# Optimization experiments

Measured on AMD Instinct MI355X. Metric: run time of the kernel, lower is better.

## Reference

```python
import jax, jax.numpy as jnp
import numpy as np

S, N, K = 8, 2048, 64          # snapshots, atoms, max neighbors (sum of max_num_neighs)
L = 20.0                        # periodic box length
R_CS, R_C = 6.0, 12.0           # smooth cutoff radii
M2 = 16                         # dim_sub_net


def _mlp(x, params, resnet=False):
    # DenseChainNet: Linear -> relu per layer; resnet skip when dims match or double (DeepMD style)
    for W, b in params:
        y = jax.nn.relu(x @ W + b)
        if resnet and y.shape[-1] == x.shape[-1]:
            y = y + x
        elif resnet and y.shape[-1] == 2 * x.shape[-1]:
            y = y + jnp.concatenate([x, x], axis=-1)
        x = y
    return x


def setup_inputs() -> dict:
    ks = jax.random.split(jax.random.key(0), 14)
    inputs = jax.random.uniform(ks[0], (S, N, 3), jnp.float32) * L
    input_types = jax.random.randint(ks[1], (S, N), 0, 2)
    nl = jax.random.randint(ks[2], (S, N, K), 0, N)
    neigh_list = jnp.where(jax.random.uniform(ks[3], (S, N, K)) < 0.2, -1, nl)  # -1 = padded neighbor

    def w(k, i, o):
        return jax.random.normal(k, (i, o), jnp.float32) / np.float32(np.sqrt(i))

    return {
        'inputs': inputs,
        'input_types': input_types,
        'neigh_list': neigh_list,
        'length': jnp.array([L, L, L], jnp.float32),
        # embed_species (species_dim [2,16,32])
        'ew0': w(ks[4], 2, 16), 'eb0': jnp.zeros((16,), jnp.float32),
        'ew1': w(ks[5], 16, 32), 'eb1': jnp.zeros((32,), jnp.float32),
        # fit_species (species_fit [32,32,31])
        'fw0': w(ks[6], 32, 32), 'fb0': jnp.zeros((32,), jnp.float32),
        'fw1': w(ks[7], 32, 31), 'fb1': jnp.zeros((31,), jnp.float32),
        # embed_net (descript_dim [32,64,128], resnet=True)
        'gw0': w(ks[8], 32, 64), 'gb0': jnp.zeros((64,), jnp.float32),
        'gw1': w(ks[9], 64, 128), 'gb1': jnp.zeros((128,), jnp.float32),
    }


def reference(inputs, input_types, neigh_list, length,
              ew0, eb0, ew1, eb1, fw0, fb0, fw1, fb1, gw0, gb0, gw1, gb1):
    mask = neigh_list == -1                                   # [S,N,K]
    idx = jnp.where(mask, 0, neigh_list)

    # ---- gen_coordinates_smooth: neighbor gather + min-image + smooth cutoff ----
    neigh_pos = jax.vmap(lambda p, i: p[i])(inputs, idx)      # [S,N,K,3]
    diff = neigh_pos - inputs[:, :, None, :]
    diff = diff - length * jnp.round(diff / length)           # minimum image convention
    rsq = jnp.sum(diff * diff, axis=-1)
    r = jnp.sqrt(jnp.where(rsq > 0, rsq, 1.0))                # safe sqrt (self/padded pairs)
    inv = 1.0 / r
    u = (r - R_CS) / (R_C - R_CS)
    sw = jnp.where(r < R_CS, inv,
                   jnp.where(r < R_C, inv * (0.5 * jnp.cos(jnp.pi * u) + 0.5), 0.0))
    valid = (~mask) & (rsq > 0)
    s_ij = jnp.where(valid, sw, 0.0)                          # [S,N,K]  s(r)
    r_ij = diff * (s_ij / r)[..., None]                       # [S,N,K,3] s(r)*x/r

    # ---- SpeciesModule: pair-type embedding (symmetrized) ----
    neigh_types = jax.vmap(lambda t, i: t[i])(input_types, idx)           # [S,N,K]
    center = jnp.broadcast_to(input_types[:, :, None], (S, N, K))
    pairs = jnp.stack([center, neigh_types], axis=-1).astype(jnp.float32).reshape(-1, 2)
    emb = [(ew0, eb0), (ew1, eb1)]
    t = _mlp(pairs, emb) + _mlp(pairs[:, ::-1], emb)
    td = _mlp(t, [(fw0, fb0), (fw1, fb1)]).reshape(S, N, K, -1)           # [S,N,K,31]
    td = jnp.where(mask[..., None], 0.0, td)

    # ---- embedding net + descriptor contraction ----
    s_tilde = jnp.concatenate([td, s_ij[..., None]], axis=-1)             # [S,N,K,32]
    G = _mlp(s_tilde.reshape(S * N * K, -1), [(gw0, gb0), (gw1, gb1)],
             resnet=True).reshape(S, N, K, -1)                            # [S,N,K,128]
    r_tilde = jnp.concatenate([s_ij[..., None], r_ij], axis=-1)           # [S,N,K,4]
    G2 = G[..., :M2]
    R = jnp.einsum('snkd,snkm->sndm', r_tilde, G2)                        # [S,N,4,16]
    R1 = jnp.einsum('snkd,sndm->snkm', r_tilde, R)                        # [S,N,K,16]
    D = jnp.einsum('snke,snkm->snem', G, R1)                              # [S,N,128,16]
    return D
```

## Files before the change

### kernel.cpp

```cpp
#include <hip/hip_runtime.h>
#include <math.h>

#define S_DIM 8
#define N_DIM 2048
#define K_DIM 64
#define APW 4
#define ST_ST 40
#define ST_H1 72

typedef __attribute__((ext_vector_type(8))) short bf16x8;
typedef __attribute__((ext_vector_type(4))) float f32x4;

__device__ __forceinline__ unsigned short f2bf(float x) {
    union { float f; unsigned u; } v; v.f = x;
    unsigned r = (v.u + 0x7FFFu + ((v.u >> 16) & 1u)) >> 16;
    return (unsigned short)r;
}
__device__ __forceinline__ float bf2f(unsigned short h) {
    union { unsigned u; float f; } v; v.u = ((unsigned)h) << 16;
    return v.f;
}
__device__ __forceinline__ f32x4 quad_reduce(f32x4 v) {
    v[0] += __shfl_xor(v[0], 16); v[1] += __shfl_xor(v[1], 16);
    v[2] += __shfl_xor(v[2], 16); v[3] += __shfl_xor(v[3], 16);
    v[0] += __shfl_xor(v[0], 32); v[1] += __shfl_xor(v[1], 32);
    v[2] += __shfl_xor(v[2], 32); v[3] += __shfl_xor(v[3], 32);
    return v;
}

__global__ __launch_bounds__(256) void prep_kernel(
        const float* __restrict__ ew0, const float* __restrict__ eb0,
        const float* __restrict__ ew1, const float* __restrict__ eb1,
        const float* __restrict__ fw0, const float* __restrict__ fb0,
        const float* __restrict__ fw1, const float* __restrict__ fb1,
        const float* __restrict__ gw0, const float* __restrict__ gw1,
        float* __restrict__ td_tab,
        unsigned short* __restrict__ w0t, unsigned short* __restrict__ w1t) {
    __shared__ float l_ew0[32], l_eb0[16], l_ew1[512], l_eb1[32];
    __shared__ float l_fw0[1024], l_fb0[32], l_fw1[992], l_fb1[31];
    __shared__ float l_h[4][2][16];
    __shared__ float l_tv[4][32];
    __shared__ float l_f1[4][32];

    const int tid = threadIdx.x;
    if (tid < 32) l_ew0[tid] = ew0[tid];
    if (tid < 16) l_eb0[tid] = eb0[tid];
    for (int i = tid; i < 512; i += 256) l_ew1[i] = ew1[i];
    if (tid < 32) l_eb1[tid] = eb1[tid];
    for (int i = tid; i < 1024; i += 256) l_fw0[i] = fw0[i];
    if (tid < 32) l_fb0[tid] = fb0[tid];
    for (int i = tid; i < 992; i += 256) l_fw1[i] = fw1[i];
    if (tid < 31) l_fb1[tid] = fb1[tid];
    __syncthreads();

    if (tid < 128) {
        const int p = tid >> 5, ord = (tid >> 4) & 1, j = tid & 15;
        const float c = (float)(p >> 1), t = (float)(p & 1);
        const float x0 = ord ? t : c;
        const float x1 = ord ? c : t;
        l_h[p][ord][j] = fmaxf(x0 * l_ew0[j] + x1 * l_ew0[16 + j] + l_eb0[j], 0.f);
    }
    __syncthreads();

    if (tid < 128) {
        const int p = tid >> 5, j = tid & 31;
        float acc = 0.f;
#pragma unroll
        for (int ord = 0; ord < 2; ord++) {
            float v = l_eb1[j];
#pragma unroll
            for (int i = 0; i < 16; i++) v += l_h[p][ord][i] * l_ew1[i * 32 + j];
            acc += fmaxf(v, 0.f);
        }
        l_tv[p][j] = acc;
    }
    __syncthreads();

    if (tid < 128) {
        const int p = tid >> 5, j = tid & 31;
        float v = l_fb0[j];
#pragma unroll
        for (int i = 0; i < 32; i++) v += l_tv[p][i] * l_fw0[i * 32 + j];
        l_f1[p][j] = fmaxf(v, 0.f);
    }
    __syncthreads();

    if (tid < 128) {
        const int p = tid >> 5, j = tid & 31;
        if (j < 31) {
            float v = l_fb1[j];
#pragma unroll
            for (int i = 0; i < 32; i++) v += l_f1[p][i] * l_fw1[i * 31 + j];
            td_tab[p * 32 + j] = fmaxf(v, 0.f);
        } else {
            td_tab[p * 32 + 31] = 0.f;
        }
    }

    for (int idx = tid; idx < 2048; idx += 256) {
        const int j = idx >> 5, i = idx & 31;
        w0t[idx] = f2bf(gw0[i * 64 + j]);
    }
    for (int idx = tid; idx < 8192; idx += 256) {
        const int e = idx >> 6, j = idx & 63;
        w1t[idx] = f2bf(gw1[j * 128 + e]);
    }
}

__global__ __launch_bounds__(64, 2) void descr_mfma(
    const float* __restrict__ inputs, const int* __restrict__ input_types,
    const int* __restrict__ neigh_list, const float* __restrict__ length,
    const float* __restrict__ gb0, const float* __restrict__ gb1,
    const float* __restrict__ td_tab, const unsigned short* __restrict__ w0t,
    const unsigned short* __restrict__ w1t, float* __restrict__ out)
{
    __shared__ __align__(16) unsigned short s_st[64 * ST_ST];
    __shared__ __align__(16) unsigned short s_h1[64 * ST_H1];
    __shared__ __align__(16) float s_rt[64 * 4];
    __shared__ __align__(16) float s_A[128 * 4];
    __shared__ __align__(16) float s_B[64 * 4];

    const int lane = threadIdx.x;
    const int l15 = lane & 15;
    const int q = lane >> 4;

    bf16x8 w0f[4];
#pragma unroll
    for (int nt = 0; nt < 4; nt++)
        w0f[nt] = *(const bf16x8*)&w0t[(nt * 16 + l15) * 32 + q * 8];
    bf16x8 w1f[8][2];
#pragma unroll
    for (int et = 0; et < 8; et++) {
        w1f[et][0] = *(const bf16x8*)&w1t[(et * 16 + l15) * 64 + q * 8];
        w1f[et][1] = *(const bf16x8*)&w1t[(et * 16 + l15) * 64 + 32 + q * 8];
    }
    float b0f[4], b1f[8];
#pragma unroll
    for (int jt = 0; jt < 4; jt++) b0f[jt] = gb0[jt * 16 + l15];
#pragma unroll
    for (int et = 0; et < 8; et++) b1f[et] = gb1[et * 16 + l15];
    const float Lx = length[0], Ly = length[1], Lz = length[2];

    for (int aa = 0; aa < APW; aa++) {
        const int atom = blockIdx.x * APW + aa;
        const int sidx = atom >> 11;

        {
            const int nb = neigh_list[atom * K_DIM + lane];
            const bool msk = nb < 0;
            const int idx = msk ? 0 : nb;
            const float cx = inputs[atom * 3 + 0];
            const float cy = inputs[atom * 3 + 1];
            const float cz = inputs[atom * 3 + 2];
            const int nbase = (sidx * N_DIM + idx) * 3;
            float dx = inputs[nbase + 0] - cx;
            float dy = inputs[nbase + 1] - cy;
            float dz = inputs[nbase + 2] - cz;
            dx -= Lx * rintf(dx / Lx);
            dy -= Ly * rintf(dy / Ly);
            dz -= Lz * rintf(dz / Lz);
            const float rsq = dx * dx + dy * dy + dz * dz;
            const float r = sqrtf(rsq > 0.f ? rsq : 1.f);
            const float inv = 1.f / r;
            float sw;
            if (r < 6.f) sw = inv;
            else if (r < 12.f) {
                const float u = (r - 6.f) * (1.f / 6.f);
                sw = inv * (0.5f * __cosf(3.14159265358979323846f * u) + 0.5f);
            } else sw = 0.f;
            const bool valid = (!msk) && (rsq > 0.f);
            const float sij = valid ? sw : 0.f;
            const float f = sij * inv;
            *(float4*)&s_rt[lane * 4] = make_float4(sij, dx * f, dy * f, dz * f);

            const int ct = input_types[atom];
            const int ntp = input_types[sidx * N_DIM + idx];
            const float* tdr = &td_tab[(ct * 2 + ntp) * 32];
            const float zm = msk ? 0.f : 1.f;
            unsigned* strow = (unsigned*)&s_st[lane * ST_ST];
#pragma unroll
            for (int i = 0; i < 16; i++) {
                const float a = tdr[2 * i] * zm;
                const float b = (i == 15) ? sij : tdr[2 * i + 1] * zm;
                strow[i] = (unsigned)f2bf(a) | ((unsigned)f2bf(b) << 16);
            }
        }
        __syncthreads();

        f32x4 Bp[4] = {{0.f,0.f,0.f,0.f},{0.f,0.f,0.f,0.f},{0.f,0.f,0.f,0.f},{0.f,0.f,0.f,0.f}};
#pragma unroll
        for (int mt = 0; mt < 4; mt++) {
            const bf16x8 afr = *(const bf16x8*)&s_st[(mt * 16 + l15) * ST_ST + q * 8];
            f32x4 c1[4];
#pragma unroll
            for (int jt = 0; jt < 4; jt++) {
                f32x4 z = {0.f, 0.f, 0.f, 0.f};
                c1[jt] = __builtin_amdgcn_mfma_f32_16x16x32_bf16(afr, w0f[jt], z, 0, 0, 0);
            }
            f32x4 rtr[4];
#pragma unroll
            for (int reg = 0; reg < 4; reg++)
                rtr[reg] = *(const f32x4*)&s_rt[(mt * 16 + q * 4 + reg) * 4];
#pragma unroll
            for (int jt = 0; jt < 4; jt++) {
                const int jcol = (jt & 1) * 16 + l15;
#pragma unroll
                for (int reg = 0; reg < 4; reg++) {
                    const int k = mt * 16 + q * 4 + reg;
                    const float h = fmaxf(c1[jt][reg] + b0f[jt], 0.f) + bf2f(s_st[k * ST_ST + jcol]);
                    Bp[jt] += h * rtr[reg];
                    s_h1[k * ST_H1 + jt * 16 + l15] = f2bf(h);
                }
            }
        }
#pragma unroll
        for (int jt = 0; jt < 4; jt++) Bp[jt] = quad_reduce(Bp[jt]);
        if (lane < 16) {
#pragma unroll
            for (int jt = 0; jt < 4; jt++)
                *(f32x4*)&s_B[(jt * 16 + lane) * 4] = Bp[jt];
        }
        __syncthreads();

        f32x4 Ap[8] = {{0.f,0.f,0.f,0.f},{0.f,0.f,0.f,0.f},{0.f,0.f,0.f,0.f},{0.f,0.f,0.f,0.f},
                       {0.f,0.f,0.f,0.f},{0.f,0.f,0.f,0.f},{0.f,0.f,0.f,0.f},{0.f,0.f,0.f,0.f}};
#pragma unroll
        for (int kt = 0; kt < 4; kt++) {
            const bf16x8 a0 = *(const bf16x8*)&s_h1[(kt * 16 + l15) * ST_H1 + q * 8];
            const bf16x8 a1 = *(const bf16x8*)&s_h1[(kt * 16 + l15) * ST_H1 + 32 + q * 8];
            f32x4 rtr[4];
#pragma unroll
            for (int reg = 0; reg < 4; reg++)
                rtr[reg] = *(const f32x4*)&s_rt[(kt * 16 + q * 4 + reg) * 4];
#pragma unroll
            for (int et = 0; et < 8; et++) {
                f32x4 c2 = {0.f, 0.f, 0.f, 0.f};
                c2 = __builtin_amdgcn_mfma_f32_16x16x32_bf16(a0, w1f[et][0], c2, 0, 0, 0);
                c2 = __builtin_amdgcn_mfma_f32_16x16x32_bf16(a1, w1f[et][1], c2, 0, 0, 0);
#pragma unroll
                for (int reg = 0; reg < 4; reg++) {
                    const float g = fmaxf(c2[reg] + b1f[et], 0.f);
                    Ap[et] += g * rtr[reg];
                }
            }
        }
#pragma unroll
        for (int et = 0; et < 8; et++) Ap[et] = quad_reduce(Ap[et]);
        if (lane < 16) {
#pragma unroll
            for (int et = 0; et < 8; et++) {
                const int e = et * 16 + lane;
                const f32x4 bb = *(const f32x4*)&s_B[(e & 63) * 4];
                const f32x4 v = Ap[et] + bb;
                *(f32x4*)&s_A[e * 4] = v;
            }
        }
        __syncthreads();

        {
            const int m0 = (lane & 3) * 4;
            const int er = lane >> 2;
            f32x4 Am[4];
#pragma unroll
            for (int t = 0; t < 4; t++) Am[t] = *(const f32x4*)&s_A[(m0 + t) * 4];
            float* op = out + (size_t)atom * 2048;
#pragma unroll
            for (int g = 0; g < 8; g++) {
                const int e = g * 16 + er;
                const f32x4 Ae = *(const f32x4*)&s_A[e * 4];
                f32x4 o;
                o[0] = Ae[0]*Am[0][0] + Ae[1]*Am[0][1] + Ae[2]*Am[0][2] + Ae[3]*Am[0][3];
                o[1] = Ae[0]*Am[1][0] + Ae[1]*Am[1][1] + Ae[2]*Am[1][2] + Ae[3]*Am[1][3];
                o[2] = Ae[0]*Am[2][0] + Ae[1]*Am[2][1] + Ae[2]*Am[2][2] + Ae[3]*Am[2][3];
                o[3] = Ae[0]*Am[3][0] + Ae[1]*Am[3][1] + Ae[2]*Am[3][2] + Ae[3]*Am[3][3];
                *(f32x4*)&op[e * 16 + m0] = o;
            }
        }
        __syncthreads();
    }
}

extern "C" void kernel_launch(void* const* d_in, const int* in_sizes, int n_in,
                              void* d_out, int out_size, void* d_ws, size_t ws_size,
                              hipStream_t stream) {
    (void)in_sizes; (void)n_in; (void)out_size; (void)ws_size;
    const float* inputs      = (const float*)d_in[0];
    const int*   input_types = (const int*)d_in[1];
    const int*   neigh_list  = (const int*)d_in[2];
    const float* length      = (const float*)d_in[3];
    const float* ew0 = (const float*)d_in[4];
    const float* eb0 = (const float*)d_in[5];
    const float* ew1 = (const float*)d_in[6];
    const float* eb1 = (const float*)d_in[7];
    const float* fw0 = (const float*)d_in[8];
    const float* fb0 = (const float*)d_in[9];
    const float* fw1 = (const float*)d_in[10];
    const float* fb1 = (const float*)d_in[11];
    const float* gw0 = (const float*)d_in[12];
    const float* gb0 = (const float*)d_in[13];
    const float* gw1 = (const float*)d_in[14];
    const float* gb1 = (const float*)d_in[15];
    float* out = (float*)d_out;

    float* td_tab = (float*)d_ws;
    unsigned short* w0t = (unsigned short*)((char*)d_ws + 512);
    unsigned short* w1t = (unsigned short*)((char*)d_ws + 512 + 4096);

    hipLaunchKernelGGL(prep_kernel, dim3(1), dim3(256), 0, stream,
                       ew0, eb0, ew1, eb1, fw0, fb0, fw1, fb1, gw0, gw1,
                       td_tab, w0t, w1t);

    const int nblocks = (S_DIM * N_DIM) / APW;
    hipLaunchKernelGGL(descr_mfma, dim3(nblocks), dim3(64), 0, stream,
                       inputs, input_types, neigh_list, length,
                       gb0, gb1, td_tab, w0t, w1t, out);
}
```

Measured before the change: 245.2 us.

## Move r_tilde contractions onto MFMA and pre-pack bf16 type table

Replaces the scalar FMA accumulation plus cross-lane shuffle reductions for the r_tilde-weighted sums over neighbors with bf16 MFMA instructions. A transposed r_tilde tile is packed as an A fragment and the activations as B fragments. The type-embedding table is pre-converted to packed bf16 in the prep kernel and staged in LDS, removing per-neighbor float-to-bf16 conversion. It also reuses s_st as the output staging buffer, replaces divides by reciprocal multiplies, and moves a barrier to the top of the loop. The trade-off is lower precision, since r_tilde and the activations are now rounded or truncated to bf16 in the contraction, and the layout juggling adds risk.

```diff
diff --git a/kernel.cpp b/kernel.cpp
--- a/kernel.cpp
+++ b/kernel.cpp
@@ -10,22 +10,30 @@
 
 typedef __attribute__((ext_vector_type(8))) short bf16x8;
 typedef __attribute__((ext_vector_type(4))) float f32x4;
-
+typedef __attribute__((ext_vector_type(4))) int   i32x4;
+
+__device__ __forceinline__ unsigned asu(float x) {
+    union { float f; unsigned u; } v; v.f = x; return v.u;
+}
 __device__ __forceinline__ unsigned short f2bf(float x) {
-    union { float f; unsigned u; } v; v.f = x;
-    unsigned r = (v.u + 0x7FFFu + ((v.u >> 16) & 1u)) >> 16;
-    return (unsigned short)r;
+    unsigned u = asu(x);
+    return (unsigned short)((u + 0x7FFFu + ((u >> 16) & 1u)) >> 16);
 }
 __device__ __forceinline__ float bf2f(unsigned short h) {
-    union { unsigned u; float f; } v; v.u = ((unsigned)h) << 16;
-    return v.f;
-}
-__device__ __forceinline__ f32x4 quad_reduce(f32x4 v) {
-    v[0] += __shfl_xor(v[0], 16); v[1] += __shfl_xor(v[1], 16);
-    v[2] += __shfl_xor(v[2], 16); v[3] += __shfl_xor(v[3], 16);
-    v[0] += __shfl_xor(v[0], 32); v[1] += __shfl_xor(v[1], 32);
-    v[2] += __shfl_xor(v[2], 32); v[3] += __shfl_xor(v[3], 32);
-    return v;
+    union { unsigned u; float f; } v; v.u = ((unsigned)h) << 16; return v.f;
+}
+__device__ __forceinline__ unsigned rne_pk(float x, float y) {
+    unsigned ux = asu(x), uy = asu(y);
+    return ((ux + 0x7FFFu + ((ux >> 16) & 1u)) >> 16) |
+           ((uy + 0x7FFFu + ((uy >> 16) & 1u)) & 0xFFFF0000u);
+}
+__device__ __forceinline__ unsigned trn_pk(float x, float y) {
+    return (asu(x) >> 16) | (asu(y) & 0xFFFF0000u);
+}
+__device__ __forceinline__ bf16x8 half_frag(unsigned p0, unsigned p1) {
+    union { i32x4 i; bf16x8 b; } u;
+    u.i = (i32x4){(int)p0, (int)p1, 0, 0};
+    return u.b;
 }
 
 __global__ __launch_bounds__(256) void prep_kernel(
@@ -34,13 +42,14 @@
         const float* __restrict__ fw0, const float* __restrict__ fb0,
         const float* __restrict__ fw1, const float* __restrict__ fb1,
         const float* __restrict__ gw0, const float* __restrict__ gw1,
-        float* __restrict__ td_tab,
+        unsigned* __restrict__ td_pk,
         unsigned short* __restrict__ w0t, unsigned short* __restrict__ w1t) {
     __shared__ float l_ew0[32], l_eb0[16], l_ew1[512], l_eb1[32];
     __shared__ float l_fw0[1024], l_fb0[32], l_fw1[992], l_fb1[31];
     __shared__ float l_h[4][2][16];
     __shared__ float l_tv[4][32];
     __shared__ float l_f1[4][32];
+    __shared__ float l_td[4][32];
 
     const int tid = threadIdx.x;
     if (tid < 32) l_ew0[tid] = ew0[tid];
@@ -61,7 +70,6 @@
         l_h[p][ord][j] = fmaxf(x0 * l_ew0[j] + x1 * l_ew0[16 + j] + l_eb0[j], 0.f);
     }
     __syncthreads();
-
     if (tid < 128) {
         const int p = tid >> 5, j = tid & 31;
         float acc = 0.f;
@@ -75,7 +83,6 @@
         l_tv[p][j] = acc;
     }
     __syncthreads();
-
     if (tid < 128) {
         const int p = tid >> 5, j = tid & 31;
         float v = l_fb0[j];
@@ -84,17 +91,23 @@
         l_f1[p][j] = fmaxf(v, 0.f);
     }
     __syncthreads();
-
     if (tid < 128) {
         const int p = tid >> 5, j = tid & 31;
         if (j < 31) {
             float v = l_fb1[j];
 #pragma unroll
             for (int i = 0; i < 32; i++) v += l_f1[p][i] * l_fw1[i * 31 + j];
-            td_tab[p * 32 + j] = fmaxf(v, 0.f);
+            l_td[p][j] = fmaxf(v, 0.f);
         } else {
-            td_tab[p * 32 + 31] = 0.f;
-        }
+            l_td[p][31] = 0.f;
+        }
+    }
+    __syncthreads();
+    if (tid < 64) {
+        const int p = tid >> 4, i = tid & 15;
+        const unsigned lo = f2bf(l_td[p][2 * i]);
+        const unsigned hi = (i == 15) ? 0u : (unsigned)f2bf(l_td[p][2 * i + 1]);
+        td_pk[tid] = lo | (hi << 16);
     }
 
     for (int idx = tid; idx < 2048; idx += 256) {
@@ -111,14 +124,14 @@
     const float* __restrict__ inputs, const int* __restrict__ input_types,
     const int* __restrict__ neigh_list, const float* __restrict__ length,
     const float* __restrict__ gb0, const float* __restrict__ gb1,
-    const float* __restrict__ td_tab, const unsigned short* __restrict__ w0t,
+    const unsigned* __restrict__ td_pk, const unsigned short* __restrict__ w0t,
     const unsigned short* __restrict__ w1t, float* __restrict__ out)
 {
     __shared__ __align__(16) unsigned short s_st[64 * ST_ST];
     __shared__ __align__(16) unsigned short s_h1[64 * ST_H1];
-    __shared__ __align__(16) float s_rt[64 * 4];
-    __shared__ __align__(16) float s_A[128 * 4];
-    __shared__ __align__(16) float s_B[64 * 4];
+    __shared__ __align__(16) float s_rtT[4 * 68];
+    __shared__ unsigned s_tdpk[64];
+    float* s_A = (float*)s_st;
 
     const int lane = threadIdx.x;
     const int l15 = lane & 15;
@@ -139,11 +152,17 @@
     for (int jt = 0; jt < 4; jt++) b0f[jt] = gb0[jt * 16 + l15];
 #pragma unroll
     for (int et = 0; et < 8; et++) b1f[et] = gb1[et * 16 + l15];
+    s_tdpk[lane] = td_pk[lane];
     const float Lx = length[0], Ly = length[1], Lz = length[2];
+    const float iLx = 1.f / Lx, iLy = 1.f / Ly, iLz = 1.f / Lz;
+
+    const f32x4 zf = {0.f, 0.f, 0.f, 0.f};
 
     for (int aa = 0; aa < APW; aa++) {
         const int atom = blockIdx.x * APW + aa;
         const int sidx = atom >> 11;
+
+        __syncthreads();
 
         {
             const int nb = neigh_list[atom * K_DIM + lane];
@@ -156,9 +175,9 @@
             float dx = inputs[nbase + 0] - cx;
             float dy = inputs[nbase + 1] - cy;
             float dz = inputs[nbase + 2] - cz;
-            dx -= Lx * rintf(dx / Lx);
-            dy -= Ly * rintf(dy / Ly);
-            dz -= Lz * rintf(dz / Lz);
+            dx -= Lx * rintf(dx * iLx);
+            dy -= Ly * rintf(dy * iLy);
+            dz -= Lz * rintf(dz * iLz);
             const float rsq = dx * dx + dy * dy + dz * dz;
             const float r = sqrtf(rsq > 0.f ? rsq : 1.f);
             const float inv = 1.f / r;
@@ -171,88 +190,77 @@
             const bool valid = (!msk) && (rsq > 0.f);
             const float sij = valid ? sw : 0.f;
             const float f = sij * inv;
-            *(float4*)&s_rt[lane * 4] = make_float4(sij, dx * f, dy * f, dz * f);
+            s_rtT[0 * 68 + lane] = sij;
+            s_rtT[1 * 68 + lane] = dx * f;
+            s_rtT[2 * 68 + lane] = dy * f;
+            s_rtT[3 * 68 + lane] = dz * f;
 
             const int ct = input_types[atom];
             const int ntp = input_types[sidx * N_DIM + idx];
-            const float* tdr = &td_tab[(ct * 2 + ntp) * 32];
-            const float zm = msk ? 0.f : 1.f;
+            const unsigned* tdr = &s_tdpk[(ct * 2 + ntp) * 16];
+            const unsigned zmask = msk ? 0u : 0xFFFFFFFFu;
             unsigned* strow = (unsigned*)&s_st[lane * ST_ST];
 #pragma unroll
-            for (int i = 0; i < 16; i++) {
-                const float a = tdr[2 * i] * zm;
-                const float b = (i == 15) ? sij : tdr[2 * i + 1] * zm;
-                strow[i] = (unsigned)f2bf(a) | ((unsigned)f2bf(b) << 16);
-            }
+            for (int i = 0; i < 15; i++) strow[i] = tdr[i] & zmask;
+            strow[15] = (tdr[15] & zmask & 0xFFFFu) | (((unsigned)f2bf(sij)) << 16);
+            strow[16] = 0; strow[17] = 0; strow[18] = 0; strow[19] = 0;
         }
         __syncthreads();
 
-        f32x4 Bp[4] = {{0.f,0.f,0.f,0.f},{0.f,0.f,0.f,0.f},{0.f,0.f,0.f,0.f},{0.f,0.f,0.f,0.f}};
+        bf16x8 rtf[4];
+#pragma unroll
+        for (int a = 0; a < 4; a++) {
+            const f32x4 rv = *(const f32x4*)&s_rtT[(l15 & 3) * 68 + a * 16 + q * 4];
+            rtf[a] = half_frag(rne_pk(rv[0], rv[1]), rne_pk(rv[2], rv[3]));
+        }
+
+        f32x4 Bj[4] = {zf, zf, zf, zf};
 #pragma unroll
         for (int mt = 0; mt < 4; mt++) {
             const bf16x8 afr = *(const bf16x8*)&s_st[(mt * 16 + l15) * ST_ST + q * 8];
             f32x4 c1[4];
 #pragma unroll
+            for (int jt = 0; jt < 4; jt++)
+                c1[jt] = __builtin_amdgcn_mfma_f32_16x16x32_bf16(afr, w0f[jt], zf, 0, 0, 0);
+#pragma unroll
             for (int jt = 0; jt < 4; jt++) {
-                f32x4 z = {0.f, 0.f, 0.f, 0.f};
-                c1[jt] = __builtin_amdgcn_mfma_f32_16x16x32_bf16(afr, w0f[jt], z, 0, 0, 0);
-            }
-            f32x4 rtr[4];
-#pragma unroll
-            for (int reg = 0; reg < 4; reg++)
-                rtr[reg] = *(const f32x4*)&s_rt[(mt * 16 + q * 4 + reg) * 4];
-#pragma unroll
-            for (int jt = 0; jt < 4; jt++) {
-                const int jcol = (jt & 1) * 16 + l15;
+                float hv[4];
 #pragma unroll
                 for (int reg = 0; reg < 4; reg++) {
                     const int k = mt * 16 + q * 4 + reg;
-                    const float h = fmaxf(c1[jt][reg] + b0f[jt], 0.f) + bf2f(s_st[k * ST_ST + jcol]);
-                    Bp[jt] += h * rtr[reg];
-                    s_h1[k * ST_H1 + jt * 16 + l15] = f2bf(h);
+                    const float r = bf2f(s_st[k * ST_ST + (jt & 1) * 16 + l15]);
+                    hv[reg] = fmaxf(c1[jt][reg] + b0f[jt], 0.f) + r;
+                    s_h1[k * ST_H1 + jt * 16 + l15] = f2bf(hv[reg]);
                 }
+                const bf16x8 hf = half_frag(trn_pk(hv[0], hv[1]), trn_pk(hv[2], hv[3]));
+                Bj[jt] = __builtin_amdgcn_mfma_f32_16x16x32_bf16(rtf[mt], hf, Bj[jt], 0, 0, 0);
             }
         }
-#pragma unroll
-        for (int jt = 0; jt < 4; jt++) Bp[jt] = quad_reduce(Bp[jt]);
-        if (lane < 16) {
-#pragma unroll
-            for (int jt = 0; jt < 4; jt++)
-                *(f32x4*)&s_B[(jt * 16 + lane) * 4] = Bp[jt];
-        }
         __syncthreads();
 
-        f32x4 Ap[8] = {{0.f,0.f,0.f,0.f},{0.f,0.f,0.f,0.f},{0.f,0.f,0.f,0.f},{0.f,0.f,0.f,0.f},
-                       {0.f,0.f,0.f,0.f},{0.f,0.f,0.f,0.f},{0.f,0.f,0.f,0.f},{0.f,0.f,0.f,0.f}};
+        f32x4 AT[8] = {zf, zf, zf, zf, zf, zf, zf, zf};
 #pragma unroll
         for (int kt = 0; kt < 4; kt++) {
             const bf16x8 a0 = *(const bf16x8*)&s_h1[(kt * 16 + l15) * ST_H1 + q * 8];
             const bf16x8 a1 = *(const bf16x8*)&s_h1[(kt * 16 + l15) * ST_H1 + 32 + q * 8];
-            f32x4 rtr[4];
-#pragma unroll
-            for (int reg = 0; reg < 4; reg++)
-                rtr[reg] = *(const f32x4*)&s_rt[(kt * 16 + q * 4 + reg) * 4];
 #pragma unroll
             for (int et = 0; et < 8; et++) {
-                f32x4 c2 = {0.f, 0.f, 0.f, 0.f};
-                c2 = __builtin_amdgcn_mfma_f32_16x16x32_bf16(a0, w1f[et][0], c2, 0, 0, 0);
+                f32x4 c2 = __builtin_amdgcn_mfma_f32_16x16x32_bf16(a0, w1f[et][0], zf, 0, 0, 0);
                 c2 = __builtin_amdgcn_mfma_f32_16x16x32_bf16(a1, w1f[et][1], c2, 0, 0, 0);
-#pragma unroll
-                for (int reg = 0; reg < 4; reg++) {
-                    const float g = fmaxf(c2[reg] + b1f[et], 0.f);
-                    Ap[et] += g * rtr[reg];
-                }
+                const float g0 = fmaxf(c2[0] + b1f[et], 0.f);
+                const float g1 = fmaxf(c2[1] + b1f[et], 0.f);
+                const float g2 = fmaxf(c2[2] + b1f[et], 0.f);
+                const float g3 = fmaxf(c2[3] + b1f[et], 0.f);
+                const bf16x8 gf = half_frag(trn_pk(g0, g1), trn_pk(g2, g3));
+                AT[et] = __builtin_amdgcn_mfma_f32_16x16x32_bf16(rtf[kt], gf, AT[et], 0, 0, 0);
             }
         }
-#pragma unroll
-        for (int et = 0; et < 8; et++) Ap[et] = quad_reduce(Ap[et]);
+
         if (lane < 16) {
 #pragma unroll
             for (int et = 0; et < 8; et++) {
-                const int e = et * 16 + lane;
-                const f32x4 bb = *(const f32x4*)&s_B[(e & 63) * 4];
-                const f32x4 v = Ap[et] + bb;
-                *(f32x4*)&s_A[e * 4] = v;
+                const f32x4 v = AT[et] + Bj[et & 3];
+                *(f32x4*)&s_A[(et * 16 + lane) * 4] = v;
             }
         }
         __syncthreads();
@@ -276,7 +284,6 @@
                 *(f32x4*)&op[e * 16 + m0] = o;
             }
         }
-        __syncthreads();
     }
 }
 
@@ -302,16 +309,16 @@
     const float* gb1 = (const float*)d_in[15];
     float* out = (float*)d_out;
 
-    float* td_tab = (float*)d_ws;
+    unsigned* td_pk = (unsigned*)d_ws;
     unsigned short* w0t = (unsigned short*)((char*)d_ws + 512);
     unsigned short* w1t = (unsigned short*)((char*)d_ws + 512 + 4096);
 
     hipLaunchKernelGGL(prep_kernel, dim3(1), dim3(256), 0, stream,
                        ew0, eb0, ew1, eb1, fw0, fb0, fw1, fb1, gw0, gw1,
-                       td_tab, w0t, w1t);
+                       td_pk, w0t, w1t);
 
     const int nblocks = (S_DIM * N_DIM) / APW;
     hipLaunchKernelGGL(descr_mfma, dim3(nblocks), dim3(64), 0, stream,
                        inputs, input_types, neigh_list, length,
-                       gb0, gb1, td_tab, w0t, w1t, out);
-}
+                       gb0, gb1, td_pk, w0t, w1t, out);
+}
```

New measurement: 229.3 us. -6.5%, faster.
